# Kernel tuning notes

Hardware: AMD Instinct MI355X
Metric: run time of the kernel (lower is better)

## Reference

```python
import jax, jax.numpy as jnp
import numpy as np

HID = 1024
HEADS = 16
HEAD_DIM = HID // HEADS
MAX_P = 64
TAB = 2 * MAX_P + 1
B, L = 8, 512


def setup_inputs() -> dict:
    key = jax.random.key(0)
    ks = jax.random.split(key, 16)
    def lin(k, fan_in, fan_out):
        lim = 1.0 / np.sqrt(fan_in)
        kw, kb = jax.random.split(k)
        W = jax.random.uniform(kw, (fan_out, fan_in), jnp.float32, -lim, lim)
        b = jax.random.uniform(kb, (fan_out,), jnp.float32, -lim, lim)
        return W, b
    Wq, bq = lin(ks[0], HID, HID)
    Wk, bk = lin(ks[1], HID, HID)
    Wv, bv = lin(ks[2], HID, HID)
    Wo, bo = lin(ks[3], HID, HID)
    # xavier_uniform for relative-position tables
    xlim = float(np.sqrt(6.0 / (TAB + HEAD_DIM)))
    table_k = jax.random.uniform(ks[4], (TAB, HEAD_DIM), jnp.float32, -xlim, xlim)
    table_v = jax.random.uniform(ks[5], (TAB, HEAD_DIM), jnp.float32, -xlim, xlim)
    return {
        "query": jax.random.normal(ks[6], (B, L, HID), jnp.float32),
        "key": jax.random.normal(ks[7], (B, L, HID), jnp.float32),
        "value": jax.random.normal(ks[8], (B, L, HID), jnp.float32),
        "final_mat": jax.random.randint(ks[9], (B, L, L), 0, TAB, jnp.int64 if jax.config.jax_enable_x64 else jnp.int32),
        "Wq": Wq, "bq": bq, "Wk": Wk, "bk": bk,
        "Wv": Wv, "bv": bv, "Wo": Wo, "bo": bo,
        "table_k": table_k, "table_v": table_v,
    }


def reference(query, key, value, final_mat, Wq, bq, Wk, bk, Wv, bv, Wo, bo, table_k, table_v):
    Bt, Lq, D = query.shape
    H, hd = HEADS, HEAD_DIM
    q = query @ Wq.T + bq          # [B,Lq,D]
    k = key @ Wk.T + bk            # [B,Lk,D]
    v = value @ Wv.T + bv          # [B,Lv,D]
    q4 = q.reshape(Bt, Lq, H, hd)
    k4 = k.reshape(Bt, -1, H, hd)
    v4 = v.reshape(Bt, -1, H, hd)
    # content-content scores
    attn1 = jnp.einsum('bqhd,bkhd->bhqk', q4, k4)
    # content-position scores via gathered relative-key embeddings [B,Lq,Lk,hd]
    rk = table_k[final_mat]
    attn2 = jnp.einsum('bqhd,bqkd->bhqk', q4, rk)
    scale = jnp.asarray(np.sqrt(hd), q.dtype)
    attn = jax.nn.softmax((attn1 + attn2) / scale, axis=-1)  # [B,H,Lq,Lk]
    # dropout p=0 (eval)
    w1 = jnp.einsum('bhqk,bkhd->bqhd', attn, v4)
    rv = table_v[final_mat]                                   # [B,Lq,Lk,hd]
    w2 = jnp.einsum('bhqk,bqkd->bqhd', attn, rv)
    x = (w1 + w2).reshape(Bt, Lq, D)
    return x @ Wo.T + bo
```

## Files before the change

### kernel.cpp

```cpp
#include <hip/hip_runtime.h>

#define HID 1024
#define HEADS 16
#define HD 64
#define TAB 129
#define QSTR 136
#define BATCH 8
#define SEQ 512

typedef unsigned int uint;
typedef unsigned short ushort;
typedef unsigned char uchar;
typedef __attribute__((ext_vector_type(4))) float f32x4;
typedef __attribute__((ext_vector_type(8))) __bf16 bf16x8;

__device__ __forceinline__ ushort f2b(float x) {
    uint b = __float_as_uint(x);
    uint r = (b + 0x7fffu + ((b >> 16) & 1u)) >> 16;
    return (ushort)r;
}
__device__ __forceinline__ uint pk(float lo, float hi) {
    return (uint)f2b(lo) | ((uint)f2b(hi) << 16);
}
__device__ __forceinline__ float b2f(ushort u) {
    return __uint_as_float(((uint)u) << 16);
}
union U16x8 { uint u[4]; bf16x8 v; ushort s[8]; uint4 q; };
__device__ __forceinline__ bf16x8 pack8(float a0, float a1, float a2, float a3,
                                        float a4, float a5, float a6, float a7) {
    U16x8 r;
    r.u[0] = pk(a0, a1); r.u[1] = pk(a2, a3);
    r.u[2] = pk(a4, a5); r.u[3] = pk(a6, a7);
    return r.v;
}

#define GL16(gp, lp) __builtin_amdgcn_global_load_lds( \
    (const __attribute__((address_space(1))) void*)(gp), \
    (__attribute__((address_space(3))) void*)(lp), 16, 0, 0)

#define LDS_BARRIER() do { \
        asm volatile("s_waitcnt lgkmcnt(0)" ::: "memory"); \
        __builtin_amdgcn_s_barrier(); \
    } while (0)

struct ConvArgs { const float* src[7]; ushort* dst[7]; };

__global__ __launch_bounds__(256) void convert_bf16(ConvArgs ca) {
    int bid = blockIdx.x;
    int ti, lb;
    if (bid < 6144) { ti = bid >> 11; lb = bid & 2047; }
    else { int r = bid - 6144; ti = 3 + (r >> 9); lb = r & 511; }
    const float* s = ca.src[ti] + (size_t)lb * 2048 + (threadIdx.x << 3);
    ushort*      d = ca.dst[ti] + (size_t)lb * 2048 + (threadIdx.x << 3);
    float4 a = *(const float4*)s;
    float4 c = *(const float4*)(s + 4);
    uint4 u;
    u.x = pk(a.x, a.y); u.y = pk(a.z, a.w);
    u.z = pk(c.x, c.y); u.w = pk(c.z, c.w);
    *(uint4*)d = u;
}

struct GemmArgs {
    const ushort* A[3];
    const ushort* W[3];
    const float*  bias[3];
    ushort*       Cb[3];
};

__global__ __launch_bounds__(256) void gemm_qkv(GemmArgs ga) {
    const int N = HID, K = HID;
    __shared__ ushort As[2][128 * 32];
    __shared__ ushort Bs[2][128 * 32];
    const int tid = threadIdx.x;
    const int bid = blockIdx.x;
    const int swz = (bid & 7) * 96 + (bid >> 3);
    const int z   = swz >> 8;
    const int rem = swz & 255;
    const int m0  = (rem >> 3) * 128;
    const int n0  = (rem & 7) * 128;
    const ushort* A = ga.A[z];
    const ushort* W = ga.W[z];

    const int w  = tid >> 6;
    const int l  = tid & 63;
    const int lr = l & 15;
    const int lg = l >> 4;
    const int wm = w >> 1;
    const int wn = w & 1;

    const int sr = tid >> 2;
    const int sc = tid & 3;
    const int g  = sc ^ ((sr >> 1) & 3);
    const ushort* Ag0 = A + (size_t)(m0 + sr)      * K + g * 8;
    const ushort* Ag1 = A + (size_t)(m0 + sr + 64) * K + g * 8;
    const ushort* Wg0 = W + (size_t)(n0 + sr)      * K + g * 8;
    const ushort* Wg1 = W + (size_t)(n0 + sr + 64) * K + g * 8;

    f32x4 acc[4][4];
#pragma unroll
    for (int mt = 0; mt < 4; ++mt)
#pragma unroll
        for (int nt = 0; nt < 4; ++nt) acc[mt][nt] = (f32x4){0.f, 0.f, 0.f, 0.f};

#define STAGE(buf, k0) do { \
        GL16(Ag0 + (k0), &As[buf][w * 512]); \
        GL16(Ag1 + (k0), &As[buf][2048 + w * 512]); \
        GL16(Wg0 + (k0), &Bs[buf][w * 512]); \
        GL16(Wg1 + (k0), &Bs[buf][2048 + w * 512]); \
    } while (0)

    const int swl = (lr >> 1) & 3;
#define COMPUTE(buf) do { \
        bf16x8 af[4], bf[4]; \
        _Pragma("unroll") \
        for (int mt = 0; mt < 4; ++mt) \
            af[mt] = *(const bf16x8*)&As[buf][(wm * 64 + mt * 16 + lr) * 32 + (lg ^ swl) * 8]; \
        _Pragma("unroll") \
        for (int nt = 0; nt < 4; ++nt) \
            bf[nt] = *(const bf16x8*)&Bs[buf][(wn * 64 + nt * 16 + lr) * 32 + (lg ^ swl) * 8]; \
        _Pragma("unroll") \
        for (int mt = 0; mt < 4; ++mt) \
            _Pragma("unroll") \
            for (int nt = 0; nt < 4; ++nt) \
                acc[mt][nt] = __builtin_amdgcn_mfma_f32_16x16x32_bf16(af[mt], bf[nt], acc[mt][nt], 0, 0, 0); \
    } while (0)

    STAGE(0, 0);
    __syncthreads();
    const int nk = K / 32;
    for (int t = 0; t < nk - 1; ++t) {
        STAGE((t + 1) & 1, (size_t)(t + 1) * 32);
        COMPUTE(t & 1);
        __syncthreads();
    }
    COMPUTE((nk - 1) & 1);

    const float* bias = ga.bias[z];
    float bv[4];
#pragma unroll
    for (int nt = 0; nt < 4; ++nt) bv[nt] = bias[n0 + wn * 64 + nt * 16 + lr];
    ushort* Cb = ga.Cb[z];
#pragma unroll
    for (int mt = 0; mt < 4; ++mt)
#pragma unroll
        for (int r4 = 0; r4 < 4; ++r4) {
            size_t m = m0 + wm * 64 + mt * 16 + lg * 4 + r4;
            ushort* crow = Cb + m * N + n0 + wn * 64 + lr;
#pragma unroll
            for (int nt = 0; nt < 4; ++nt)
                crow[nt * 16] = f2b(acc[mt][nt][r4] + bv[nt]);
        }
#undef STAGE
#undef COMPUTE
}

__global__ __launch_bounds__(256) void gemm_wo(const ushort* __restrict__ A,
                                               const ushort* __restrict__ W,
                                               const float* __restrict__ bias,
                                               float* __restrict__ Cf) {
    const int N = HID, K = HID;
    __shared__ ushort As[2][128 * 32];
    __shared__ ushort Bs[2][64 * 32];
    const int tid = threadIdx.x;
    const int bid = blockIdx.x;
    const int swz = (bid & 7) * 64 + (bid >> 3);
    const int m0 = (swz >> 4) * 128;
    const int n0 = (swz & 15) * 64;

    const int w  = tid >> 6;
    const int l  = tid & 63;
    const int lr = l & 15;
    const int lg = l >> 4;
    const int wm = w >> 1;
    const int wn = w & 1;

    const int sr = tid >> 2;
    const int sc = tid & 3;
    const int g  = sc ^ ((sr >> 1) & 3);
    const ushort* Ag0 = A + (size_t)(m0 + sr)      * K + g * 8;
    const ushort* Ag1 = A + (size_t)(m0 + sr + 64) * K + g * 8;
    const ushort* Wg0 = W + (size_t)(n0 + sr)      * K + g * 8;

    f32x4 acc[4][2];
#pragma unroll
    for (int mt = 0; mt < 4; ++mt)
#pragma unroll
        for (int nt = 0; nt < 2; ++nt) acc[mt][nt] = (f32x4){0.f, 0.f, 0.f, 0.f};

#define STAGE(buf, k0) do { \
        GL16(Ag0 + (k0), &As[buf][w * 512]); \
        GL16(Ag1 + (k0), &As[buf][2048 + w * 512]); \
        GL16(Wg0 + (k0), &Bs[buf][w * 512]); \
    } while (0)

    const int swl = (lr >> 1) & 3;
#define COMPUTE(buf) do { \
        bf16x8 af[4], bf[2]; \
        _Pragma("unroll") \
        for (int mt = 0; mt < 4; ++mt) \
            af[mt] = *(const bf16x8*)&As[buf][(wm * 64 + mt * 16 + lr) * 32 + (lg ^ swl) * 8]; \
        _Pragma("unroll") \
        for (int nt = 0; nt < 2; ++nt) \
            bf[nt] = *(const bf16x8*)&Bs[buf][(wn * 32 + nt * 16 + lr) * 32 + (lg ^ swl) * 8]; \
        _Pragma("unroll") \
        for (int mt = 0; mt < 4; ++mt) \
            _Pragma("unroll") \
            for (int nt = 0; nt < 2; ++nt) \
                acc[mt][nt] = __builtin_amdgcn_mfma_f32_16x16x32_bf16(af[mt], bf[nt], acc[mt][nt], 0, 0, 0); \
    } while (0)

    STAGE(0, 0);
    __syncthreads();
    const int nk = K / 32;
    for (int t = 0; t < nk - 1; ++t) {
        STAGE((t + 1) & 1, (size_t)(t + 1) * 32);
        COMPUTE(t & 1);
        __syncthreads();
    }
    COMPUTE((nk - 1) & 1);

    float bv[2];
#pragma unroll
    for (int nt = 0; nt < 2; ++nt) bv[nt] = bias[n0 + wn * 32 + nt * 16 + lr];
#pragma unroll
    for (int mt = 0; mt < 4; ++mt)
#pragma unroll
        for (int r4 = 0; r4 < 4; ++r4) {
            size_t m = m0 + wm * 64 + mt * 16 + lg * 4 + r4;
            float* crow = Cf + m * N + n0 + wn * 32 + lr;
#pragma unroll
            for (int nt = 0; nt < 2; ++nt)
                crow[nt * 16] = acc[mt][nt][r4] + bv[nt];
        }
#undef STAGE
#undef COMPUTE
}

__global__ __launch_bounds__(256) void prep_kernel(const ushort* __restrict__ qb,
                                                   const float* __restrict__ table_k,
                                                   const ushort* __restrict__ vb,
                                                   const float* __restrict__ table_v,
                                                   const int* __restrict__ fmat,
                                                   ushort* __restrict__ qtab,
                                                   ushort* __restrict__ vT,
                                                   ushort* __restrict__ tvT2,
                                                   uchar* __restrict__ fm8) {
    __shared__ __align__(16) ushort shmem[144 * 72];
    const int wg  = blockIdx.x;
    const int tid = threadIdx.x;

    if (wg < 256) {
        const int h    = wg & 15;
        const int half = (wg >> 4) & 1;
        const int b    = wg >> 5;
        const int q0   = half * 256;
        ushort* tk = shmem;
        for (int i = tid; i < TAB * 8; i += 256) {
            int row = i >> 3, gr = i & 7;
            const float* src = table_k + row * HD + gr * 8;
            float4 a = *(const float4*)src;
            float4 c = *(const float4*)(src + 4);
            uint4 u;
            u.x = pk(a.x, a.y); u.y = pk(a.z, a.w);
            u.z = pk(c.x, c.y); u.w = pk(c.z, c.w);
            *(uint4*)&tk[row * 72 + gr * 8] = u;
        }
        __syncthreads();

        const int w  = tid >> 6;
        const int l  = tid & 63;
        const int lr = l & 15;
        const int lg = l >> 4;
        bf16x8 qf[4][2];
#pragma unroll
        for (int qt = 0; qt < 4; ++qt) {
            const ushort* qrow = qb + ((size_t)(b * SEQ) + q0 + w * 64 + qt * 16 + lr) * HID + h * HD;
            qf[qt][0] = *(const bf16x8*)(qrow + lg * 8);
            qf[qt][1] = *(const bf16x8*)(qrow + 32 + lg * 8);
        }
        ushort* outbase = qtab + ((size_t)(b * HEADS + h) * SEQ + q0 + w * 64) * QSTR;
#pragma unroll
        for (int mt = 0; mt < 9; ++mt) {
            bf16x8 tf0 = *(const bf16x8*)&tk[(mt * 16 + lr) * 72 + lg * 8];
            bf16x8 tf1 = *(const bf16x8*)&tk[(mt * 16 + lr) * 72 + 32 + lg * 8];
#pragma unroll
            for (int qt = 0; qt < 4; ++qt) {
                f32x4 acc = (f32x4){0.f, 0.f, 0.f, 0.f};
                acc = __builtin_amdgcn_mfma_f32_16x16x32_bf16(tf0, qf[qt][0], acc, 0, 0, 0);
                acc = __builtin_amdgcn_mfma_f32_16x16x32_bf16(tf1, qf[qt][1], acc, 0, 0, 0);
                ushort* orow = outbase + (size_t)(qt * 16 + lr) * QSTR;
                if (mt < 8) {
                    uint2 pu;
                    pu.x = pk(acc[0], acc[1]); pu.y = pk(acc[2], acc[3]);
                    *(uint2*)&orow[mt * 16 + lg * 4] = pu;
                } else if (lg == 0) {
                    orow[128] = f2b(acc[0]);
                }
            }
        }
    } else if (wg < 768) {
        const int vw = wg - 256;
        ushort* tile = shmem;
        const int b = vw >> 6, h = (vw >> 2) & 15, kc = vw & 3;
        const int k0 = kc * 128;
        {
            const int kr = tid >> 1, dc = (tid & 1) * 32;
            const ushort* src = vb + ((size_t)(b * SEQ) + k0 + kr) * HID + h * 64 + dc;
#pragma unroll
            for (int j = 0; j < 4; ++j) {
                uint4 u = *(const uint4*)(src + j * 8);
                *(uint4*)&tile[kr * 72 + dc + j * 8] = u;
            }
        }
        __syncthreads();
        {
            const int dr = tid >> 2, kc2 = (tid & 3) * 32;
            ushort* dst = vT + ((size_t)(b * 16 + h) * 64 + dr) * 512 + k0 + kc2;
#pragma unroll
            for (int j = 0; j < 4; ++j) {
                U16x8 o;
#pragma unroll
                for (int i = 0; i < 8; ++i)
                    o.s[i] = tile[(kc2 + j * 8 + i) * 72 + dr];
                *(uint4*)(dst + j * 8) = o.q;
            }
        }
    } else if (wg == 768) {
        for (int i = tid; i < 64 * 160; i += 256) {
            int d = i / 160;
            int c = i - d * 160;
            tvT2[i] = (c < TAB) ? f2b(table_v[(size_t)c * HD + d]) : (ushort)0;
        }
    } else {
        const size_t base = (size_t)(wg - 769) * 2048 + (size_t)tid * 8;
        int4 a = *(const int4*)(fmat + base);
        int4 c = *(const int4*)(fmat + base + 4);
        uint lo = (uint)a.x | ((uint)a.y << 8) | ((uint)a.z << 16) | ((uint)a.w << 24);
        uint hi = (uint)c.x | ((uint)c.y << 8) | ((uint)c.z << 16) | ((uint)c.w << 24);
        uint2 o; o.x = lo; o.y = hi;
        *(uint2*)(fm8 + base) = o;
    }
}

__global__ __launch_bounds__(256) void qk_gemm(const ushort* __restrict__ qb,
                                               const ushort* __restrict__ kb,
                                               ushort* __restrict__ S) {
    __shared__ ushort As[2][128 * 32];
    __shared__ ushort Bs[2][128 * 32];
    const int tid = threadIdx.x;
    const int m0 = blockIdx.x * 128;
    const int n0 = blockIdx.y * 128;
    const int bh = blockIdx.z;
    const int b = bh >> 4, h = bh & 15;
    const size_t rowQ = (size_t)b * SEQ;

    const int w  = tid >> 6;
    const int l  = tid & 63;
    const int lr = l & 15;
    const int lg = l >> 4;
    const int wm = w >> 1;
    const int wn = w & 1;

    const int sr = tid >> 2;
    const int sc = tid & 3;
    const int g  = sc ^ ((sr >> 1) & 3);
    const ushort* Ag0 = qb + (rowQ + m0 + sr)      * HID + h * HD + g * 8;
    const ushort* Ag1 = qb + (rowQ + m0 + sr + 64) * HID + h * HD + g * 8;
    const ushort* Wg0 = kb + (rowQ + n0 + sr)      * HID + h * HD + g * 8;
    const ushort* Wg1 = kb + (rowQ + n0 + sr + 64) * HID + h * HD + g * 8;

    GL16(Ag0,      &As[0][w * 512]); GL16(Ag1,      &As[0][2048 + w * 512]);
    GL16(Wg0,      &Bs[0][w * 512]); GL16(Wg1,      &Bs[0][2048 + w * 512]);
    GL16(Ag0 + 32, &As[1][w * 512]); GL16(Ag1 + 32, &As[1][2048 + w * 512]);
    GL16(Wg0 + 32, &Bs[1][w * 512]); GL16(Wg1 + 32, &Bs[1][2048 + w * 512]);

    f32x4 acc[4][4];
#pragma unroll
    for (int mt = 0; mt < 4; ++mt)
#pragma unroll
        for (int nt = 0; nt < 4; ++nt) acc[mt][nt] = (f32x4){0.f, 0.f, 0.f, 0.f};

    const int swl = (lr >> 1) & 3;
    __syncthreads();
#pragma unroll
    for (int buf = 0; buf < 2; ++buf) {
        bf16x8 af[4], bf[4];
#pragma unroll
        for (int mt = 0; mt < 4; ++mt)
            af[mt] = *(const bf16x8*)&As[buf][(wm * 64 + mt * 16 + lr) * 32 + (lg ^ swl) * 8];
#pragma unroll
        for (int nt = 0; nt < 4; ++nt)
            bf[nt] = *(const bf16x8*)&Bs[buf][(wn * 64 + nt * 16 + lr) * 32 + (lg ^ swl) * 8];
#pragma unroll
        for (int mt = 0; mt < 4; ++mt)
#pragma unroll
            for (int nt = 0; nt < 4; ++nt)
                acc[mt][nt] = __builtin_amdgcn_mfma_f32_16x16x32_bf16(af[mt], bf[nt], acc[mt][nt], 0, 0, 0);
    }

    ushort* Sb = S + (size_t)bh * SEQ * SEQ;
#pragma unroll
    for (int mt = 0; mt < 4; ++mt)
#pragma unroll
        for (int r4 = 0; r4 < 4; ++r4) {
            int m = m0 + wm * 64 + mt * 16 + lg * 4 + r4;
            ushort* srow = Sb + (size_t)m * SEQ + n0 + wn * 64 + lr;
#pragma unroll
            for (int nt = 0; nt < 4; ++nt)
                srow[nt * 16] = f2b(acc[mt][nt][r4]);
        }
}

__global__ __launch_bounds__(512, 4) void smpv_kernel(const ushort* __restrict__ S,
                                                      const uchar* __restrict__ fm8,
                                                      const ushort* __restrict__ qt,
                                                      const ushort* __restrict__ vT,
                                                      const ushort* __restrict__ tvT2,
                                                      ushort* __restrict__ x) {
    constexpr float FIX = 65536.0f;
    constexpr float INV_FIX = 1.0f / 65536.0f;
    __shared__ __align__(16) uint   bins[64 * 132];
    __shared__ __align__(16) ushort qtb[64 * QSTR];
    __shared__ float rowsum[2][64];

    const int tid = threadIdx.x;
    const int w   = tid >> 6;
    const int l   = tid & 63;
    const int lr  = l & 15;
    const int lg  = l >> 4;
    const int rg  = w & 3;
    const int kh  = w >> 2;

    const int bid = blockIdx.x;
    const int swz = (bid & 7) * 128 + (bid >> 3);
    const int bh  = swz >> 3;
    const int m0  = (swz & 7) * 64;
    const int b   = bh >> 4, h = bh & 15;

    {
        const uint4* src = (const uint4*)(qt + ((size_t)bh * SEQ + m0) * QSTR);
        uint4* dst = (uint4*)qtb;
        for (int i = tid; i < 64 * QSTR / 8; i += 512) dst[i] = src[i];
    }
    {
        uint4 z = {0u, 0u, 0u, 0u};
        uint4* dz = (uint4*)bins;
        for (int i = tid; i < 64 * 132 / 4; i += 512) dz[i] = z;
    }
    LDS_BARRIER();

    const int myrow = rg * 16 + lr;
    const int kbase = kh * 256;
    const ushort* Srow  = S + ((size_t)bh * SEQ + m0 + myrow) * SEQ + kbase;
    const uchar*  fmrow = fm8 + ((size_t)(b * SEQ) + m0 + myrow) * SEQ + kbase;
    const ushort* qrow  = qtb + myrow * QSTR;
    uint*         brow  = bins + myrow * 132;
    const ushort* vbase = vT + (size_t)bh * 64 * 512 + kbase;

    U16x8 sv[8];
    uint2 fmv[8];
#pragma unroll
    for (int i = 0; i < 8; ++i) {
        const int k0 = i * 32 + lg * 8;
        sv[i].q = *(const uint4*)(Srow + k0);
        fmv[i]  = *(const uint2*)(fmrow + k0);
    }
    __builtin_amdgcn_sched_barrier(0);

    f32x4 acc[4];
#pragma unroll
    for (int nt = 0; nt < 4; ++nt) acc[nt] = (f32x4){0.f, 0.f, 0.f, 0.f};
    float lsum = 0.f;
    bf16x8 paf[8];
#pragma unroll
    for (int i = 0; i < 8; ++i) {
        const uint2 fm = fmv[i];
        int ts[8];
        ts[0] = fm.x & 255; ts[1] = (fm.x >> 8) & 255;
        ts[2] = (fm.x >> 16) & 255; ts[3] = fm.x >> 24;
        ts[4] = fm.y & 255; ts[5] = (fm.y >> 8) & 255;
        ts[6] = (fm.y >> 16) & 255; ts[7] = fm.y >> 24;
        float p[8];
#pragma unroll
        for (int j = 0; j < 8; ++j) {
            p[j] = __expf((b2f(sv[i].s[j]) + b2f(qrow[ts[j]])) * 0.125f);
            lsum += p[j];
        }
#pragma unroll
        for (int j = 0; j < 8; ++j)
            __hip_atomic_fetch_add(&brow[ts[j]], (uint)(p[j] * FIX),
                                   __ATOMIC_RELAXED, __HIP_MEMORY_SCOPE_WORKGROUP);
        paf[i] = pack8(p[0], p[1], p[2], p[3], p[4], p[5], p[6], p[7]);
    }
    lsum += __shfl_xor(lsum, 16);
    lsum += __shfl_xor(lsum, 32);
    if (lg == 0) rowsum[kh][myrow] = lsum;

#pragma unroll
    for (int i = 0; i < 8; ++i) {
        const int k0 = i * 32 + lg * 8;
#pragma unroll
        for (int nt = 0; nt < 4; ++nt) {
            bf16x8 bf_ = *(const bf16x8*)(vbase + (size_t)(nt * 16 + lr) * 512 + k0);
            acc[nt] = __builtin_amdgcn_mfma_f32_16x16x32_bf16(paf[i], bf_, acc[nt], 0, 0, 0);
        }
    }

    LDS_BARRIER();

#pragma unroll
    for (int c = 0; c < 2; ++c) {
        const int t0 = (kh * 2 + c) * 32 + lg * 8;
        const uint* bp = brow + t0;
        bf16x8 af = pack8((float)bp[0] * INV_FIX, (float)bp[1] * INV_FIX,
                          (float)bp[2] * INV_FIX, (float)bp[3] * INV_FIX,
                          (float)bp[4] * INV_FIX, (float)bp[5] * INV_FIX,
                          (float)bp[6] * INV_FIX, (float)bp[7] * INV_FIX);
#pragma unroll
        for (int nt = 0; nt < 4; ++nt) {
            bf16x8 bf_ = *(const bf16x8*)(tvT2 + (size_t)(nt * 16 + lr) * 160 + t0);
            acc[nt] = __builtin_amdgcn_mfma_f32_16x16x32_bf16(af, bf_, acc[nt], 0, 0, 0);
        }
    }

    float* obuf = (float*)qtb;
    if (kh == 1) {
#pragma unroll
        for (int nt = 0; nt < 4; ++nt)
            *(f32x4*)&obuf[((rg * 4 + nt) * 64 + l) * 4] = acc[nt];
    }
    LDS_BARRIER();

    if (kh == 0) {
#pragma unroll
        for (int nt = 0; nt < 4; ++nt) {
            f32x4 p_ = *(const f32x4*)&obuf[((rg * 4 + nt) * 64 + l) * 4];
            acc[nt][0] += p_[0]; acc[nt][1] += p_[1];
            acc[nt][2] += p_[2]; acc[nt][3] += p_[3];
        }
        float iv[4], nb[4];
#pragma unroll
        for (int r = 0; r < 4; ++r) {
            const int crow = rg * 16 + lg * 4 + r;
            iv[r] = 1.f / (rowsum[0][crow] + rowsum[1][crow]);
            nb[r] = (float)bins[crow * 132 + 128] * INV_FIX;
        }
#pragma unroll
        for (int nt = 0; nt < 4; ++nt) {
            float tv = b2f(tvT2[(size_t)(nt * 16 + lr) * 160 + 128]);
#pragma unroll
            for (int r = 0; r < 4; ++r)
                acc[nt][r] = (acc[nt][r] + nb[r] * tv) * iv[r];
        }
        ushort* orow = x + ((size_t)(b * SEQ) + m0 + rg * 16 + lg * 4) * HID + h * HD;
#pragma unroll
        for (int r = 0; r < 4; ++r)
#pragma unroll
            for (int nt = 0; nt < 4; ++nt)
                orow[(size_t)r * HID + nt * 16 + lr] = f2b(acc[nt][r]);
    }
}

extern "C" void kernel_launch(void* const* d_in, const int* in_sizes, int n_in,
                              void* d_out, int out_size, void* d_ws, size_t ws_size,
                              hipStream_t stream) {
    const float* query = (const float*)d_in[0];
    const float* key   = (const float*)d_in[1];
    const float* value = (const float*)d_in[2];
    const int*   fmat  = (const int*)d_in[3];
    const float* Wq = (const float*)d_in[4];
    const float* bq = (const float*)d_in[5];
    const float* Wk = (const float*)d_in[6];
    const float* bk = (const float*)d_in[7];
    const float* Wv = (const float*)d_in[8];
    const float* bv = (const float*)d_in[9];
    const float* Wo = (const float*)d_in[10];
    const float* bo = (const float*)d_in[11];
    const float* table_k = (const float*)d_in[12];
    const float* table_v = (const float*)d_in[13];

    const size_t nBLD = (size_t)BATCH * SEQ * HID;
    const size_t nW   = (size_t)HID * HID;
    ushort* us = (ushort*)d_ws;
    ushort* qin16 = us;                 us += nBLD;
    ushort* kin16 = us;                 us += nBLD;
    ushort* vin16 = us;                 us += nBLD;
    ushort* wq16  = us;                 us += nW;
    ushort* wk16  = us;                 us += nW;
    ushort* wv16  = us;                 us += nW;
    ushort* wo16  = us;                 us += nW;
    ushort* qb16  = us;                 us += nBLD;
    ushort* kb16  = us;                 us += nBLD;
    ushort* vb16  = us;                 us += nBLD;
    ushort* qt16  = us;                 us += (size_t)BATCH * HEADS * SEQ * QSTR;
    ushort* xb16  = us;                 us += nBLD;
    uchar*  fm8   = (uchar*)us;         us += (size_t)BATCH * SEQ * SEQ / 2;
    ushort* Sbuf  = us;                 us += (size_t)BATCH * HEADS * SEQ * SEQ;

    ConvArgs ca;
    ca.src[0] = query; ca.src[1] = key; ca.src[2] = value;
    ca.src[3] = Wq; ca.src[4] = Wk; ca.src[5] = Wv; ca.src[6] = Wo;
    ca.dst[0] = qin16; ca.dst[1] = kin16; ca.dst[2] = vin16;
    ca.dst[3] = wq16; ca.dst[4] = wk16; ca.dst[5] = wv16; ca.dst[6] = wo16;
    convert_bf16<<<dim3(8192), 256, 0, stream>>>(ca);

    GemmArgs gq = {};
    gq.A[0] = qin16; gq.A[1] = kin16; gq.A[2] = vin16;
    gq.W[0] = wq16;  gq.W[1] = wk16;  gq.W[2] = wv16;
    gq.bias[0] = bq; gq.bias[1] = bk; gq.bias[2] = bv;
    gq.Cb[0] = qb16; gq.Cb[1] = kb16; gq.Cb[2] = vb16;
    gemm_qkv<<<dim3(768), 256, 0, stream>>>(gq);

    ushort* vTbuf  = qin16;
    ushort* tvTbuf = kin16;

    prep_kernel<<<dim3(1793), 256, 0, stream>>>(qb16, table_k, vb16, table_v,
                                                fmat, qt16, vTbuf, tvTbuf, fm8);

    qk_gemm<<<dim3(4, 4, 128), 256, 0, stream>>>(qb16, kb16, Sbuf);
    smpv_kernel<<<dim3(1024), 512, 0, stream>>>(Sbuf, fm8, qt16, vTbuf, tvTbuf, xb16);

    gemm_wo<<<dim3(512), 256, 0, stream>>>(xb16, wo16, bo, (float*)d_out);
}
```

Measured before the change: 167.3 us.

## Fuse relative-key bias gather and exp into QK GEMM epilogue

```diff
diff --git a/kernel.cpp b/kernel.cpp
--- a/kernel.cpp
+++ b/kernel.cpp
@@ -273,10 +273,10 @@
         const int lg = l >> 4;
         bf16x8 qf[4][2];
 #pragma unroll
-        for (int qt = 0; qt < 4; ++qt) {
-            const ushort* qrow = qb + ((size_t)(b * SEQ) + q0 + w * 64 + qt * 16 + lr) * HID + h * HD;
-            qf[qt][0] = *(const bf16x8*)(qrow + lg * 8);
-            qf[qt][1] = *(const bf16x8*)(qrow + 32 + lg * 8);
+        for (int qt_ = 0; qt_ < 4; ++qt_) {
+            const ushort* qrow = qb + ((size_t)(b * SEQ) + q0 + w * 64 + qt_ * 16 + lr) * HID + h * HD;
+            qf[qt_][0] = *(const bf16x8*)(qrow + lg * 8);
+            qf[qt_][1] = *(const bf16x8*)(qrow + 32 + lg * 8);
         }
         ushort* outbase = qtab + ((size_t)(b * HEADS + h) * SEQ + q0 + w * 64) * QSTR;
 #pragma unroll
@@ -284,11 +284,11 @@
             bf16x8 tf0 = *(const bf16x8*)&tk[(mt * 16 + lr) * 72 + lg * 8];
             bf16x8 tf1 = *(const bf16x8*)&tk[(mt * 16 + lr) * 72 + 32 + lg * 8];
 #pragma unroll
-            for (int qt = 0; qt < 4; ++qt) {
+            for (int qt_ = 0; qt_ < 4; ++qt_) {
                 f32x4 acc = (f32x4){0.f, 0.f, 0.f, 0.f};
-                acc = __builtin_amdgcn_mfma_f32_16x16x32_bf16(tf0, qf[qt][0], acc, 0, 0, 0);
-                acc = __builtin_amdgcn_mfma_f32_16x16x32_bf16(tf1, qf[qt][1], acc, 0, 0, 0);
-                ushort* orow = outbase + (size_t)(qt * 16 + lr) * QSTR;
+                acc = __builtin_amdgcn_mfma_f32_16x16x32_bf16(tf0, qf[qt_][0], acc, 0, 0, 0);
+                acc = __builtin_amdgcn_mfma_f32_16x16x32_bf16(tf1, qf[qt_][1], acc, 0, 0, 0);
+                ushort* orow = outbase + (size_t)(qt_ * 16 + lr) * QSTR;
                 if (mt < 8) {
                     uint2 pu;
                     pu.x = pk(acc[0], acc[1]); pu.y = pk(acc[2], acc[3]);
@@ -342,11 +342,14 @@
     }
 }
 
-__global__ __launch_bounds__(256) void qk_gemm(const ushort* __restrict__ qb,
-                                               const ushort* __restrict__ kb,
-                                               ushort* __restrict__ S) {
-    __shared__ ushort As[2][128 * 32];
-    __shared__ ushort Bs[2][128 * 32];
+__global__ __launch_bounds__(256) void qkp_gemm(const ushort* __restrict__ qb,
+                                                const ushort* __restrict__ kb,
+                                                const ushort* __restrict__ qt,
+                                                const uchar* __restrict__ fm8,
+                                                ushort* __restrict__ P) {
+    __shared__ __align__(16) ushort sh[128 * QSTR];
+    ushort* As = sh;
+    ushort* Bs = sh + 8192;
     const int tid = threadIdx.x;
     const int m0 = blockIdx.x * 128;
     const int n0 = blockIdx.y * 128;
@@ -369,10 +372,10 @@
     const ushort* Wg0 = kb + (rowQ + n0 + sr)      * HID + h * HD + g * 8;
     const ushort* Wg1 = kb + (rowQ + n0 + sr + 64) * HID + h * HD + g * 8;
 
-    GL16(Ag0,      &As[0][w * 512]); GL16(Ag1,      &As[0][2048 + w * 512]);
-    GL16(Wg0,      &Bs[0][w * 512]); GL16(Wg1,      &Bs[0][2048 + w * 512]);
-    GL16(Ag0 + 32, &As[1][w * 512]); GL16(Ag1 + 32, &As[1][2048 + w * 512]);
-    GL16(Wg0 + 32, &Bs[1][w * 512]); GL16(Wg1 + 32, &Bs[1][2048 + w * 512]);
+    GL16(Ag0,      &As[0 * 4096 + w * 512]); GL16(Ag1,      &As[0 * 4096 + 2048 + w * 512]);
+    GL16(Wg0,      &Bs[0 * 4096 + w * 512]); GL16(Wg1,      &Bs[0 * 4096 + 2048 + w * 512]);
+    GL16(Ag0 + 32, &As[1 * 4096 + w * 512]); GL16(Ag1 + 32, &As[1 * 4096 + 2048 + w * 512]);
+    GL16(Wg0 + 32, &Bs[1 * 4096 + w * 512]); GL16(Wg1 + 32, &Bs[1 * 4096 + 2048 + w * 512]);
 
     f32x4 acc[4][4];
 #pragma unroll
@@ -387,10 +390,10 @@
         bf16x8 af[4], bf[4];
 #pragma unroll
         for (int mt = 0; mt < 4; ++mt)
-            af[mt] = *(const bf16x8*)&As[buf][(wm * 64 + mt * 16 + lr) * 32 + (lg ^ swl) * 8];
+            af[mt] = *(const bf16x8*)&As[buf * 4096 + (wm * 64 + mt * 16 + lr) * 32 + (lg ^ swl) * 8];
 #pragma unroll
         for (int nt = 0; nt < 4; ++nt)
-            bf[nt] = *(const bf16x8*)&Bs[buf][(wn * 64 + nt * 16 + lr) * 32 + (lg ^ swl) * 8];
+            bf[nt] = *(const bf16x8*)&Bs[buf * 4096 + (wn * 64 + nt * 16 + lr) * 32 + (lg ^ swl) * 8];
 #pragma unroll
         for (int mt = 0; mt < 4; ++mt)
 #pragma unroll
@@ -398,29 +401,41 @@
                 acc[mt][nt] = __builtin_amdgcn_mfma_f32_16x16x32_bf16(af[mt], bf[nt], acc[mt][nt], 0, 0, 0);
     }
 
-    ushort* Sb = S + (size_t)bh * SEQ * SEQ;
+    __syncthreads();
+    {
+        const uint4* src = (const uint4*)(qt + ((size_t)bh * SEQ + m0) * QSTR);
+        uint4* dst = (uint4*)sh;
+        for (int i = tid; i < 128 * QSTR / 8; i += 256) dst[i] = src[i];
+    }
+    __syncthreads();
+
+    ushort* Pb = P + (size_t)bh * SEQ * SEQ;
 #pragma unroll
     for (int mt = 0; mt < 4; ++mt)
 #pragma unroll
         for (int r4 = 0; r4 < 4; ++r4) {
-            int m = m0 + wm * 64 + mt * 16 + lg * 4 + r4;
-            ushort* srow = Sb + (size_t)m * SEQ + n0 + wn * 64 + lr;
-#pragma unroll
-            for (int nt = 0; nt < 4; ++nt)
-                srow[nt * 16] = f2b(acc[mt][nt][r4]);
-        }
-}
-
-__global__ __launch_bounds__(512, 4) void smpv_kernel(const ushort* __restrict__ S,
+            const int mloc = wm * 64 + mt * 16 + lg * 4 + r4;
+            const int m = m0 + mloc;
+            const uchar* fr = fm8 + ((size_t)(b * SEQ) + m) * SEQ + n0 + wn * 64 + lr;
+            ushort* prow = Pb + (size_t)m * SEQ + n0 + wn * 64 + lr;
+#pragma unroll
+            for (int nt = 0; nt < 4; ++nt) {
+                const int t = fr[nt * 16];
+                float p = __expf((acc[mt][nt][r4] + b2f(sh[mloc * QSTR + t])) * 0.125f);
+                prow[nt * 16] = f2b(p);
+            }
+        }
+}
+
+__global__ __launch_bounds__(512, 4) void smpv_kernel(const ushort* __restrict__ P,
                                                       const uchar* __restrict__ fm8,
-                                                      const ushort* __restrict__ qt,
                                                       const ushort* __restrict__ vT,
                                                       const ushort* __restrict__ tvT2,
                                                       ushort* __restrict__ x) {
     constexpr float FIX = 65536.0f;
     constexpr float INV_FIX = 1.0f / 65536.0f;
-    __shared__ __align__(16) uint   bins[64 * 132];
-    __shared__ __align__(16) ushort qtb[64 * QSTR];
+    __shared__ __align__(16) uint  bins[64 * 132];
+    __shared__ __align__(16) float obuf[4096];
     __shared__ float rowsum[2][64];
 
     const int tid = threadIdx.x;
@@ -438,11 +453,6 @@
     const int b   = bh >> 4, h = bh & 15;
 
     {
-        const uint4* src = (const uint4*)(qt + ((size_t)bh * SEQ + m0) * QSTR);
-        uint4* dst = (uint4*)qtb;
-        for (int i = tid; i < 64 * QSTR / 8; i += 512) dst[i] = src[i];
-    }
-    {
         uint4 z = {0u, 0u, 0u, 0u};
         uint4* dz = (uint4*)bins;
         for (int i = tid; i < 64 * 132 / 4; i += 512) dz[i] = z;
@@ -451,9 +461,8 @@
 
     const int myrow = rg * 16 + lr;
     const int kbase = kh * 256;
-    const ushort* Srow  = S + ((size_t)bh * SEQ + m0 + myrow) * SEQ + kbase;
+    const ushort* Prow  = P + ((size_t)bh * SEQ + m0 + myrow) * SEQ + kbase;
     const uchar*  fmrow = fm8 + ((size_t)(b * SEQ) + m0 + myrow) * SEQ + kbase;
-    const ushort* qrow  = qtb + myrow * QSTR;
     uint*         brow  = bins + myrow * 132;
     const ushort* vbase = vT + (size_t)bh * 64 * 512 + kbase;
 
@@ -462,16 +471,12 @@
 #pragma unroll
     for (int i = 0; i < 8; ++i) {
         const int k0 = i * 32 + lg * 8;
-        sv[i].q = *(const uint4*)(Srow + k0);
+        sv[i].q = *(const uint4*)(Prow + k0);
         fmv[i]  = *(const uint2*)(fmrow + k0);
     }
     __builtin_amdgcn_sched_barrier(0);
 
-    f32x4 acc[4];
-#pragma unroll
-    for (int nt = 0; nt < 4; ++nt) acc[nt] = (f32x4){0.f, 0.f, 0.f, 0.f};
     float lsum = 0.f;
-    bf16x8 paf[8];
 #pragma unroll
     for (int i = 0; i < 8; ++i) {
         const uint2 fm = fmv[i];
@@ -480,29 +485,28 @@
         ts[2] = (fm.x >> 16) & 255; ts[3] = fm.x >> 24;
         ts[4] = fm.y & 255; ts[5] = (fm.y >> 8) & 255;
         ts[6] = (fm.y >> 16) & 255; ts[7] = fm.y >> 24;
-        float p[8];
 #pragma unroll
         for (int j = 0; j < 8; ++j) {
-            p[j] = __expf((b2f(sv[i].s[j]) + b2f(qrow[ts[j]])) * 0.125f);
-            lsum += p[j];
-        }
-#pragma unroll
-        for (int j = 0; j < 8; ++j)
-            __hip_atomic_fetch_add(&brow[ts[j]], (uint)(p[j] * FIX),
+            float pj = b2f(sv[i].s[j]);
+            lsum += pj;
+            __hip_atomic_fetch_add(&brow[ts[j]], (uint)(pj * FIX),
                                    __ATOMIC_RELAXED, __HIP_MEMORY_SCOPE_WORKGROUP);
-        paf[i] = pack8(p[0], p[1], p[2], p[3], p[4], p[5], p[6], p[7]);
+        }
     }
     lsum += __shfl_xor(lsum, 16);
     lsum += __shfl_xor(lsum, 32);
     if (lg == 0) rowsum[kh][myrow] = lsum;
 
+    f32x4 acc[4];
+#pragma unroll
+    for (int nt = 0; nt < 4; ++nt) acc[nt] = (f32x4){0.f, 0.f, 0.f, 0.f};
 #pragma unroll
     for (int i = 0; i < 8; ++i) {
         const int k0 = i * 32 + lg * 8;
 #pragma unroll
         for (int nt = 0; nt < 4; ++nt) {
             bf16x8 bf_ = *(const bf16x8*)(vbase + (size_t)(nt * 16 + lr) * 512 + k0);
-            acc[nt] = __builtin_amdgcn_mfma_f32_16x16x32_bf16(paf[i], bf_, acc[nt], 0, 0, 0);
+            acc[nt] = __builtin_amdgcn_mfma_f32_16x16x32_bf16(sv[i].v, bf_, acc[nt], 0, 0, 0);
         }
     }
 
@@ -523,7 +527,6 @@
         }
     }
 
-    float* obuf = (float*)qtb;
     if (kh == 1) {
 #pragma unroll
         for (int nt = 0; nt < 4; ++nt)
@@ -617,8 +620,8 @@
     prep_kernel<<<dim3(1793), 256, 0, stream>>>(qb16, table_k, vb16, table_v,
                                                 fmat, qt16, vTbuf, tvTbuf, fm8);
 
-    qk_gemm<<<dim3(4, 4, 128), 256, 0, stream>>>(qb16, kb16, Sbuf);
-    smpv_kernel<<<dim3(1024), 512, 0, stream>>>(Sbuf, fm8, qt16, vTbuf, tvTbuf, xb16);
+    qkp_gemm<<<dim3(4, 4, 128), 256, 0, stream>>>(qb16, kb16, qt16, fm8, Sbuf);
+    smpv_kernel<<<dim3(1024), 512, 0, stream>>>(Sbuf, fm8, vTbuf, tvTbuf, xb16);
 
     gemm_wo<<<dim3(512), 256, 0, stream>>>(xb16, wo16, bo, (float*)d_out);
 }
```

After: 176.5 us. 1.05x slower.
